# Kernel tuning notes

Measured on AMD Instinct MI355X. Metric: run time of the kernel, lower is better.

The kernel has to match this reference:

```python
import jax, jax.numpy as jnp
import numpy as np

H = 128  # lstm hidden

def _lstm_layer(x_tbi, Wih, Whh, bih, bhh):
    # x_tbi: [T, B, I]; Wih: [4H, I]; Whh: [4H, H]; biases: [4H]
    T, B, _ = x_tbi.shape
    b = bih + bhh
    # precompute input projections for all timesteps: [T, B, 4H]
    x_proj = jnp.einsum('tbi,gi->tbg', x_tbi, Wih) + b
    def step(carry, xp):
        h, c = carry
        gates = xp + h @ Whh.T  # [B, 4H]
        i, f, g, o = jnp.split(gates, 4, axis=-1)  # torch gate order i,f,g,o
        i = jax.nn.sigmoid(i); f = jax.nn.sigmoid(f)
        g = jnp.tanh(g); o = jax.nn.sigmoid(o)
        c = f * c + i * g
        h = o * jnp.tanh(c)
        return (h, c), h
    h0 = jnp.zeros((B, H), x_tbi.dtype)
    c0 = jnp.zeros((B, H), x_tbi.dtype)
    (_, _), hs = jax.lax.scan(step, (h0, c0), x_proj)
    return hs  # [T, B, H]


def setup_inputs() -> dict:
    key = jax.random.key(0)
    ks = jax.random.split(key, 14)
    B, T, I = 256, 512, 30
    k = 1.0 / np.sqrt(H)
    u = lambda kk, shape: jax.random.uniform(kk, shape, jnp.float32, -k, k)
    return {
        'x':    jax.random.normal(ks[0], (B, T, I), jnp.float32),
        'Wih0': u(ks[1], (4 * H, I)),
        'Whh0': u(ks[2], (4 * H, H)),
        'bih0': u(ks[3], (4 * H,)),
        'bhh0': u(ks[4], (4 * H,)),
        'Wih1': u(ks[5], (4 * H, H)),
        'Whh1': u(ks[6], (4 * H, H)),
        'bih1': u(ks[7], (4 * H,)),
        'bhh1': u(ks[8], (4 * H,)),
        'Wl':   u(ks[9], (84, H)),
        'bl':   u(ks[10], (84,)),
        'Wo':   u(ks[11], (63, 84)),
        'bo':   u(ks[12], (63,)),
    }


def reference(x, Wih0, Whh0, bih0, bhh0, Wih1, Whh1, bih1, bhh1, Wl, bl, Wo, bo):
    # x: [B, T, 30] -> time-major for scan
    x_tbi = jnp.swapaxes(x, 0, 1)
    h1 = _lstm_layer(x_tbi, Wih0, Whh0, bih0, bhh0)   # [T, B, H]
    h2 = _lstm_layer(h1,    Wih1, Whh1, bih1, bhh1)   # [T, B, H]
    y = jnp.swapaxes(h2, 0, 1)                         # [B, T, H]
    y = y @ Wl.T + bl                                  # [B, T, 84]
    out = y @ Wo.T + bo                                # [B, T, 63]
    return out
```

## Files before the change

kernel.cpp:

```cpp
#include <hip/hip_runtime.h>
#include <hip/hip_fp16.h>

#define B_ 256
#define T_ 512
#define H_ 128
#define M_ (B_ * T_)

typedef _Float16 f16x8 __attribute__((ext_vector_type(8)));
typedef float    f32x4 __attribute__((ext_vector_type(4)));

__device__ __forceinline__ float rcp_f(float a) { return __builtin_amdgcn_rcpf(a); }
__device__ __forceinline__ float sigmoid_f(float a) { return rcp_f(1.f + __expf(-a)); }
__device__ __forceinline__ float tanh_f(float a) { return 1.f - 2.f * rcp_f(__expf(2.f * a) + 1.f); }

__device__ __forceinline__ void lds_barrier() {
    asm volatile("s_waitcnt lgkmcnt(0)\n\ts_barrier" ::: "memory");
}

#define PINV(X) asm volatile("" : "+v"(X))

__device__ __forceinline__ __half cell_update(float g0, float g1, float g2, float g3, float& c) {
    float iv = sigmoid_f(g0), fv = sigmoid_f(g1);
    float gv = tanh_f(g2),   ov = sigmoid_f(g3);
    c = fv * c + iv * gv;
    return __float2half(ov * tanh_f(c));
}

__device__ __forceinline__ void store_dwordx2_sc(uint64_t addr, uint2 v) {
    asm volatile("global_store_dwordx2 %0, %1, off sc0 sc1" :: "v"(addr), "v"(v) : "memory");
}
__device__ __forceinline__ void store_flag_sc(uint64_t addr, unsigned v) {
    asm volatile("global_store_dword %0, %1, off sc0 sc1" :: "v"(addr), "v"(v) : "memory");
}
__device__ __forceinline__ unsigned load_flag_sc(uint64_t addr) {
    unsigned v;
    asm volatile("global_load_dword %0, %1, off sc0 sc1\n\ts_waitcnt vmcnt(0)"
                 : "=v"(v) : "v"(addr) : "memory");
    return v;
}
#define LOAD8_SC(dst, addr) \
    asm volatile("global_load_dwordx2 %0, %1, off sc0 sc1" : "=&v"(dst) : "v"(addr) : "memory")

__device__ __forceinline__ void poll_min8(uint64_t base, unsigned target, int lane) {
    for (;;) {
        unsigned v = 0xFFFFFFFFu;
        if (lane < 8) v = load_flag_sc(base + (uint64_t)lane * 4);
        v = min(v, (unsigned)__shfl_xor((int)v, 1));
        v = min(v, (unsigned)__shfl_xor((int)v, 2));
        v = min(v, (unsigned)__shfl_xor((int)v, 4));
        unsigned seen = (unsigned)__shfl((int)v, 0);
        if (seen >= target) break;
        __builtin_amdgcn_s_sleep(8);
    }
}

#define MFMA16(A, BV, C) __builtin_amdgcn_mfma_f32_16x16x32_f16((A), (BV), (C), 0, 0, 0)
#define MF4(AV, WARR, KT) \
    ac0 = MFMA16(AV, WARR[0][KT], ac0); \
    ac1 = MFMA16(AV, WARR[1][KT], ac1); \
    ac2 = MFMA16(AV, WARR[2][KT], ac2); \
    ac3 = MFMA16(AV, WARR[3][KT], ac3);
#define PF4(AV, KT) \
    px0 = MFMA16(AV, wi[0][KT], px0); \
    px1 = MFMA16(AV, wi[1][KT], px1); \
    px2 = MFMA16(AV, wi[2][KT], px2); \
    px3 = MFMA16(AV, wi[3][KT], px3);

__global__ __launch_bounds__(256)
void convert_kernel(const float* __restrict__ Wih0, const float* __restrict__ bih0, const float* __restrict__ bhh0,
                    const float* __restrict__ Whh0, const float* __restrict__ Wih1, const float* __restrict__ Whh1,
                    const float* __restrict__ bih1, const float* __restrict__ bhh1,
                    const float* __restrict__ Wl, const float* __restrict__ bl,
                    const float* __restrict__ Wo, const float* __restrict__ bo,
                    __half* __restrict__ W0b, __half* __restrict__ W1b,
                    __half* __restrict__ Whh0h, __half* __restrict__ Whh1h,
                    __half* __restrict__ Wc16, float* __restrict__ b0, float* __restrict__ b1,
                    float* __restrict__ bc)
{
    const int tid = threadIdx.x, bid = blockIdx.x;
    if (bid == 0) {
        for (int i = tid; i < 512; i += 256) { b0[i] = bih0[i] + bhh0[i]; b1[i] = bih1[i] + bhh1[i]; }
        for (int i = tid; i < 512 * 32; i += 256) {
            int r = i >> 5, k = i & 31;
            W0b[i] = __float2half(k < 30 ? Wih0[r * 30 + k] : 0.f);
        }
        if (tid < 64) {
            float a = 0.f;
            if (tid < 63) { a = bo[tid]; for (int m = 0; m < 84; ++m) a += Wo[tid * 84 + m] * bl[m]; }
            bc[tid] = a;
        }
    } else if (bid <= 4) {
        const int base = (bid - 1) * 16384;
        for (int i = tid; i < 16384; i += 256) W1b[base + i] = __float2half(Wih1[base + i]);
    } else if (bid <= 8) {
        const int base = (bid - 5) * 16384;
        for (int i = tid; i < 16384; i += 256) Whh0h[base + i] = __float2half(Whh0[base + i]);
    } else if (bid <= 12) {
        const int base = (bid - 9) * 16384;
        for (int i = tid; i < 16384; i += 256) Whh1h[base + i] = __float2half(Whh1[base + i]);
    } else {
        const int base = (bid - 13) * 2048;
        for (int i = tid; i < 2048; i += 256) {
            int idx = base + i;
            int j = idx >> 7, k = idx & 127;
            float a = 0.f;
            if (j < 63) for (int m = 0; m < 84; ++m) a += Wo[j * 84 + m] * Wl[m * 128 + k];
            Wc16[idx] = __float2half(a);
        }
    }
}

__global__ __launch_bounds__(512, 2)
void lstm_fused(const float* __restrict__ x,
                const __half* __restrict__ W0b, const __half* __restrict__ Whh0h,
                const __half* __restrict__ W1b, const __half* __restrict__ Whh1h,
                const float* __restrict__ b0, const float* __restrict__ b1,
                __half* __restrict__ xp, __half* __restrict__ h2g,
                unsigned* __restrict__ flags)
{
    const int bid = blockIdx.x;
    const bool producer = bid < 128;
    const int g = producer ? bid : bid - 128;
    const int tid = threadIdx.x;
    const int w = tid >> 6;
    const int lane = tid & 63;
    const int l15 = lane & 15, qg = lane >> 4;
    const int j = w * 16 + l15;
    const int r = l15 >> 2;

    __shared__ __align__(16) char hist[32 * 1280];
    __shared__ __align__(16) char hbuf_s[2][1280];
    __shared__ __align__(16) __half xl[2][129][32];
    char* const hb0 = hbuf_s[0];
    char* const hb1 = hbuf_s[1];

    const int ro0 = r * 320 + 0 * 64 + qg * 16;
    const int ro1 = r * 320 + 1 * 64 + qg * 16;
    const int ro2 = r * 320 + 2 * 64 + qg * 16;
    const int ro3 = r * 320 + 3 * 64 + qg * 16;
    const int wo  = qg * 320 + j * 2;

    for (int i = tid; i < 10240; i += 512) ((unsigned*)hist)[i] = 0;
    for (int i = tid; i < 320; i += 512) ((unsigned*)hb0)[i] = 0;

    const uint64_t fb = (uint64_t)(uintptr_t)flags;
    const uint64_t flagbase = fb + (uint64_t)(g * 8) * 4;
    float c = 0.f;

    if (producer) {
        float bias4[4], b14[4];
        f16x8 wx[4], wb[4][4], wi[4][4];
#pragma unroll
        for (int q = 0; q < 4; ++q) {
            bias4[q] = b0[q * 128 + j];
            b14[q]   = b1[q * 128 + j];
            wx[q] = *reinterpret_cast<const f16x8*>(W0b + (size_t)(q * 128 + j) * 32 + qg * 8);
            PINV(wx[q]); PINV(bias4[q]); PINV(b14[q]);
#pragma unroll
            for (int kt = 0; kt < 4; ++kt) {
                wb[q][kt] = *reinterpret_cast<const f16x8*>(Whh0h + (size_t)(q * 128 + j) * 128 + kt * 32 + qg * 8);
                wi[q][kt] = *reinterpret_cast<const f16x8*>(W1b   + (size_t)(q * 128 + j) * 128 + kt * 32 + qg * 8);
                PINV(wb[q][kt]); PINV(wi[q][kt]);
            }
        }
        for (int idx = tid; idx < 512; idx += 512) {
            int b4 = idx >> 8, rest = idx & 255;
            xl[b4][rest >> 1][30 + (rest & 1)] = __float2half(0.f);
        }
        if (tid < 512) {
            int idx = tid;
            if (idx < 512) {
                int b4 = idx >> 8, rest = idx & 255;
                xl[b4][rest >> 1][30 + (rest & 1)] = __float2half(0.f);
            }
        }
        const uint64_t pflag = flagbase + (uint64_t)w * 4;
        const uint64_t xpj = (uint64_t)(uintptr_t)xp + ((uint64_t)(4 * j) << 1);
        const char* xlb = (const char*)xl;
        const int xro = (r & 1) * 8256 + qg * 16;
        __syncthreads();

        auto xp1_gemm = [&](int cc2) {
#pragma unroll
            for (int rt = 0; rt < 4; ++rt) {
                const int row = rt * 16 + l15;
                const char* ap = hist + (((cc2 * 16 + (row >> 2)) & 31) * 1280 + (row & 3) * 320 + qg * 16);
                f16x8 h0_ = *(const f16x8*)(ap + 0);
                f16x8 h1_ = *(const f16x8*)(ap + 64);
                f16x8 h2_ = *(const f16x8*)(ap + 128);
                f16x8 h3_ = *(const f16x8*)(ap + 192);
                f32x4 px0 = (f32x4){b14[0], b14[0], b14[0], b14[0]};
                f32x4 px1 = (f32x4){b14[1], b14[1], b14[1], b14[1]};
                f32x4 px2 = (f32x4){b14[2], b14[2], b14[2], b14[2]};
                f32x4 px3 = (f32x4){b14[3], b14[3], b14[3], b14[3]};
                PF4(h0_, 0) PF4(h1_, 1) PF4(h2_, 2) PF4(h3_, 3)
#pragma unroll
                for (int r4 = 0; r4 < 4; ++r4) {
                    const int ro_ = rt * 16 + qg * 4 + r4;
                    const int tglob = cc2 * 16 + (ro_ >> 2);
                    const int b2 = ro_ & 3;
                    if (b2 < 2) {
                        __half2 lo_ = __floats2half2_rn(px0[r4], px1[r4]);
                        __half2 hi_ = __floats2half2_rn(px2[r4], px3[r4]);
                        uint2 pk_;
                        pk_.x = __builtin_bit_cast(unsigned, lo_);
                        pk_.y = __builtin_bit_cast(unsigned, hi_);
                        store_dwordx2_sc(xpj + ((uint64_t)((g * 2 + b2) * T_ + tglob) << 10), pk_);
                    }
                }
            }
        };

#define PSTEP(TT) do {                                                          \
        const int t_ = (TT);                                                    \
        const char* rp_ = hist + (((t_ + 31) & 31) * 1280);                     \
        f16x8 a0_ = *(const f16x8*)(rp_ + ro0);                                 \
        f16x8 a1_ = *(const f16x8*)(rp_ + ro1);                                 \
        f16x8 a2_ = *(const f16x8*)(rp_ + ro2);                                 \
        f16x8 a3_ = *(const f16x8*)(rp_ + ro3);                                 \
        f16x8 ax_ = *(const f16x8*)(xlb + (xro + (t_ & 127) * 64));             \
        f32x4 ac0 = (f32x4){bias4[0], 0.f, 0.f, 0.f};                           \
        f32x4 ac1 = (f32x4){bias4[1], 0.f, 0.f, 0.f};                           \
        f32x4 ac2 = (f32x4){bias4[2], 0.f, 0.f, 0.f};                           \
        f32x4 ac3 = (f32x4){bias4[3], 0.f, 0.f, 0.f};                           \
        ac0 = MFMA16(ax_, wx[0], ac0); ac1 = MFMA16(ax_, wx[1], ac1);           \
        ac2 = MFMA16(ax_, wx[2], ac2); ac3 = MFMA16(ax_, wx[3], ac3);           \
        MF4(a0_, wb, 0) MF4(a1_, wb, 1) MF4(a2_, wb, 2) MF4(a3_, wb, 3)         \
        __half hh_ = cell_update(ac0[0], ac1[0], ac2[0], ac3[0], c);            \
        *(__half*)(hist + ((t_ & 31) * 1280 + qg * 320 + j * 2)) = hh_;         \
        if ((t_ & 7) == 7) {                                                    \
            asm volatile("s_waitcnt vmcnt(0)" ::: "memory");                    \
            if (lane == 0) store_flag_sc(pflag, (unsigned)(t_ + 1));            \
        }                                                                       \
        lds_barrier();                                                          \
    } while (0)

        for (int xc = 0; xc < 4; ++xc) {
#pragma unroll 1
            for (int b4 = 0; b4 < 2; ++b4) {
                const float* src = x + ((size_t)(g * 2 + b4) * T_ + xc * 128) * 30;
                for (int idx = tid; idx < 3840; idx += 512) {
                    int tt = idx / 30, ii = idx - tt * 30;
                    xl[b4][tt][ii] = __float2half(src[idx]);
                }
            }
            __syncthreads();
#pragma unroll 1
            for (int sc = 0; sc < 8; ++sc) {
                const int cc = xc * 8 + sc;
                if (cc > 0) xp1_gemm(cc - 1);
                const int tb = cc * 16;
                PSTEP(tb + 0);  PSTEP(tb + 1);  PSTEP(tb + 2);  PSTEP(tb + 3);
                PSTEP(tb + 4);  PSTEP(tb + 5);  PSTEP(tb + 6);  PSTEP(tb + 7);
                PSTEP(tb + 8);  PSTEP(tb + 9);  PSTEP(tb + 10); PSTEP(tb + 11);
                PSTEP(tb + 12); PSTEP(tb + 13); PSTEP(tb + 14); PSTEP(tb + 15);
            }
        }
        xp1_gemm(31);
        asm volatile("s_waitcnt vmcnt(0)" ::: "memory");
        if (lane == 0) store_flag_sc(pflag, 999u);
    } else {
        f16x8 wb[4][4];
#pragma unroll
        for (int q = 0; q < 4; ++q)
#pragma unroll
            for (int kt = 0; kt < 4; ++kt) {
                wb[q][kt] = *reinterpret_cast<const f16x8*>(Whh1h + (size_t)(q * 128 + j) * 128 + kt * 32 + qg * 8);
                PINV(wb[q][kt]);
            }
        const int b = g * 2 + (qg & 1);
        const bool wrl = qg < 2;
        const uint64_t xpcb = (uint64_t)(uintptr_t)xp + ((uint64_t)(((size_t)b * T_) * 512 + 4 * j) << 1);
        __half* h2p = h2g + ((size_t)b * T_) * H_ + j;
        uint2 xq0, xq1, xq2, xq3, xq4, xq5, xq6, xq7;
        __syncthreads();

#define CSTEP(TT, XQ) do {                                                      \
        const int t_ = (TT);                                                    \
        const char* rp_ = (t_ & 1) ? hb1 : hb0;                                 \
        char* wp_ = (t_ & 1) ? hb0 : hb1;                                       \
        asm volatile("s_waitcnt vmcnt(15)" ::: "memory");                       \
        __builtin_amdgcn_sched_barrier(0);                                      \
        float2 flo = __half22float2(__builtin_bit_cast(__half2, XQ.x));         \
        float2 fhi = __half22float2(__builtin_bit_cast(__half2, XQ.y));         \
        LOAD8_SC(XQ, xpcb + (uint64_t)(t_ + 8) * 1024);                         \
        f16x8 a0_ = *(const f16x8*)(rp_ + ro0);                                 \
        f16x8 a1_ = *(const f16x8*)(rp_ + ro1);                                 \
        f16x8 a2_ = *(const f16x8*)(rp_ + ro2);                                 \
        f16x8 a3_ = *(const f16x8*)(rp_ + ro3);                                 \
        f32x4 ac0 = (f32x4){flo.x, 0.f, 0.f, 0.f};                              \
        f32x4 ac1 = (f32x4){flo.y, 0.f, 0.f, 0.f};                              \
        f32x4 ac2 = (f32x4){fhi.x, 0.f, 0.f, 0.f};                              \
        f32x4 ac3 = (f32x4){fhi.y, 0.f, 0.f, 0.f};                              \
        MF4(a0_, wb, 0) MF4(a1_, wb, 1) MF4(a2_, wb, 2) MF4(a3_, wb, 3)         \
        __half hh_ = cell_update(ac0[0], ac1[0], ac2[0], ac3[0], c);            \
        *(__half*)(wp_ + wo) = hh_;                                             \
        if (wrl) h2p[(size_t)t_ * H_] = hh_;                                    \
        lds_barrier();                                                          \
    } while (0)

        for (int tg = 0; tg < T_; tg += 16) {
            unsigned target = (tg + 40 <= 512) ? (unsigned)(tg + 40) : 999u;
            poll_min8(flagbase, target, lane);
            if (tg == 0) {
                LOAD8_SC(xq0, xpcb + 0 * 1024); LOAD8_SC(xq1, xpcb + 1 * 1024);
                LOAD8_SC(xq2, xpcb + 2 * 1024); LOAD8_SC(xq3, xpcb + 3 * 1024);
                LOAD8_SC(xq4, xpcb + 4 * 1024); LOAD8_SC(xq5, xpcb + 5 * 1024);
                LOAD8_SC(xq6, xpcb + 6 * 1024); LOAD8_SC(xq7, xpcb + 7 * 1024);
                asm volatile("s_waitcnt vmcnt(0)" ::: "memory");
                __builtin_amdgcn_sched_barrier(0);
            }
            CSTEP(tg + 0, xq0);  CSTEP(tg + 1, xq1);  CSTEP(tg + 2, xq2);  CSTEP(tg + 3, xq3);
            CSTEP(tg + 4, xq4);  CSTEP(tg + 5, xq5);  CSTEP(tg + 6, xq6);  CSTEP(tg + 7, xq7);
            CSTEP(tg + 8, xq0);  CSTEP(tg + 9, xq1);  CSTEP(tg + 10, xq2); CSTEP(tg + 11, xq3);
            CSTEP(tg + 12, xq4); CSTEP(tg + 13, xq5); CSTEP(tg + 14, xq6); CSTEP(tg + 15, xq7);
        }
    }
}

__global__ __launch_bounds__(256, 4)
void head_kernel(const __half* __restrict__ in, const __half* __restrict__ W16,
                 const float* __restrict__ bias, float* __restrict__ outp)
{
    constexpr int KK = 128;
    const int lane = threadIdx.x & 63;
    const int wn = threadIdx.x >> 6;
    const int rowbase = blockIdx.x * 64;
    const int colbase = wn * 16;
    const int l15 = lane & 15, lk = (lane >> 4) * 8;

    float bcol = bias[colbase + l15];
    f32x4 acc[4];
#pragma unroll
    for (int rt = 0; rt < 4; ++rt) acc[rt] = (f32x4){0.f, 0.f, 0.f, 0.f};

#pragma unroll
    for (int kt = 0; kt < 4; ++kt) {
        f16x8 bv = *reinterpret_cast<const f16x8*>(W16 + (size_t)(colbase + l15) * KK + kt * 32 + lk);
#pragma unroll
        for (int rt = 0; rt < 4; ++rt) {
            f16x8 a = *reinterpret_cast<const f16x8*>(in + (size_t)(rowbase + rt * 16 + l15) * KK + kt * 32 + lk);
            acc[rt] = __builtin_amdgcn_mfma_f32_16x16x32_f16(a, bv, acc[rt], 0, 0, 0);
        }
    }
    const int col = colbase + l15;
#pragma unroll
    for (int rt = 0; rt < 4; ++rt)
#pragma unroll
        for (int rr = 0; rr < 4; ++rr) {
            const int row = rowbase + rt * 16 + (lane >> 4) * 4 + rr;
            if (col < 63) outp[(size_t)row * 63 + col] = acc[rt][rr] + bcol;
        }
}

extern "C" void kernel_launch(void* const* d_in, const int* in_sizes, int n_in,
                              void* d_out, int out_size, void* d_ws, size_t ws_size,
                              hipStream_t stream)
{
    const float* x    = (const float*)d_in[0];
    const float* Wih0 = (const float*)d_in[1];
    const float* Whh0 = (const float*)d_in[2];
    const float* bih0 = (const float*)d_in[3];
    const float* bhh0 = (const float*)d_in[4];
    const float* Wih1 = (const float*)d_in[5];
    const float* Whh1 = (const float*)d_in[6];
    const float* bih1 = (const float*)d_in[7];
    const float* bhh1 = (const float*)d_in[8];
    const float* Wl   = (const float*)d_in[9];
    const float* bl   = (const float*)d_in[10];
    const float* Wo   = (const float*)d_in[11];
    const float* bo   = (const float*)d_in[12];
    float* out = (float*)d_out;

    char* ws = (char*)d_ws;
    size_t off = 0;
    auto carve = [&](size_t bytes) { void* p = ws + off; off += (bytes + 255) & ~(size_t)255; return p; };
    __half* xp    = (__half*)carve((size_t)M_ * 512 * 2 + 16384);
    __half* h2    = (__half*)carve((size_t)M_ * 128 * 2);
    __half* W0b   = (__half*)carve(512 * 32 * 2);
    __half* W1b   = (__half*)carve(512 * 128 * 2);
    __half* Whh0h = (__half*)carve(512 * 128 * 2);
    __half* Whh1h = (__half*)carve(512 * 128 * 2);
    __half* Wc16  = (__half*)carve(64 * 128 * 2);
    float*  b0    = (float*)carve(512 * 4);
    float*  b1    = (float*)carve(512 * 4);
    float*  bc    = (float*)carve(64 * 4);
    unsigned* flags = (unsigned*)carve(2048 * 4);

    hipLaunchKernelGGL(convert_kernel, dim3(17), dim3(256), 0, stream,
                       Wih0, bih0, bhh0, Whh0, Wih1, Whh1, bih1, bhh1, Wl, bl, Wo, bo,
                       W0b, W1b, Whh0h, Whh1h, Wc16, b0, b1, bc);

    hipMemsetAsync(flags, 0, 2048 * 4, stream);

    hipLaunchKernelGGL(lstm_fused, dim3(256), dim3(512), 0, stream,
                       x, W0b, Whh0h, W1b, Whh1h, b0, b1, xp, h2, flags);

    hipLaunchKernelGGL(head_kernel, dim3(M_ / 64), dim3(256), 0, stream,
                       h2, Wc16, bc, out);
}
```

Before: 364.0 us.

## Precompute layer-0 input projection for step pairs ahead, shrink hidden history ring

```diff
diff --git a/kernel.cpp b/kernel.cpp
--- a/kernel.cpp
+++ b/kernel.cpp
@@ -128,9 +128,10 @@
     const int j = w * 16 + l15;
     const int r = l15 >> 2;
 
-    __shared__ __align__(16) char hist[32 * 1280];
+    __shared__ __align__(16) char hist[16 * 1280];
     __shared__ __align__(16) char hbuf_s[2][1280];
     __shared__ __align__(16) __half xl[2][129][32];
+    __shared__ __align__(16) char gb0[2 * 8 * 1040];
     char* const hb0 = hbuf_s[0];
     char* const hb1 = hbuf_s[1];
 
@@ -140,7 +141,7 @@
     const int ro3 = r * 320 + 3 * 64 + qg * 16;
     const int wo  = qg * 320 + j * 2;
 
-    for (int i = tid; i < 10240; i += 512) ((unsigned*)hist)[i] = 0;
+    for (int i = tid; i < 5120; i += 512) ((unsigned*)hist)[i] = 0;
     for (int i = tid; i < 320; i += 512) ((unsigned*)hb0)[i] = 0;
 
     const uint64_t fb = (uint64_t)(uintptr_t)flags;
@@ -167,24 +168,17 @@
             int b4 = idx >> 8, rest = idx & 255;
             xl[b4][rest >> 1][30 + (rest & 1)] = __float2half(0.f);
         }
-        if (tid < 512) {
-            int idx = tid;
-            if (idx < 512) {
-                int b4 = idx >> 8, rest = idx & 255;
-                xl[b4][rest >> 1][30 + (rest & 1)] = __float2half(0.f);
-            }
-        }
         const uint64_t pflag = flagbase + (uint64_t)w * 4;
         const uint64_t xpj = (uint64_t)(uintptr_t)xp + ((uint64_t)(4 * j) << 1);
         const char* xlb = (const char*)xl;
-        const int xro = (r & 1) * 8256 + qg * 16;
         __syncthreads();
 
         auto xp1_gemm = [&](int cc2) {
 #pragma unroll
-            for (int rt = 0; rt < 4; ++rt) {
+            for (int rt = 0; rt < 2; ++rt) {
                 const int row = rt * 16 + l15;
-                const char* ap = hist + (((cc2 * 16 + (row >> 2)) & 31) * 1280 + (row & 3) * 320 + qg * 16);
+                const int s_ = row >> 1, b2_ = row & 1;
+                const char* ap = hist + (((cc2 * 16 + s_) & 15) * 1280 + b2_ * 320 + qg * 16);
                 f16x8 h0_ = *(const f16x8*)(ap + 0);
                 f16x8 h1_ = *(const f16x8*)(ap + 64);
                 f16x8 h2_ = *(const f16x8*)(ap + 128);
@@ -197,42 +191,68 @@
 #pragma unroll
                 for (int r4 = 0; r4 < 4; ++r4) {
                     const int ro_ = rt * 16 + qg * 4 + r4;
-                    const int tglob = cc2 * 16 + (ro_ >> 2);
-                    const int b2 = ro_ & 3;
-                    if (b2 < 2) {
-                        __half2 lo_ = __floats2half2_rn(px0[r4], px1[r4]);
-                        __half2 hi_ = __floats2half2_rn(px2[r4], px3[r4]);
-                        uint2 pk_;
-                        pk_.x = __builtin_bit_cast(unsigned, lo_);
-                        pk_.y = __builtin_bit_cast(unsigned, hi_);
-                        store_dwordx2_sc(xpj + ((uint64_t)((g * 2 + b2) * T_ + tglob) << 10), pk_);
-                    }
+                    const int s2 = ro_ >> 1, b2 = ro_ & 1;
+                    __half2 lo_ = __floats2half2_rn(px0[r4], px1[r4]);
+                    __half2 hi_ = __floats2half2_rn(px2[r4], px3[r4]);
+                    uint2 pk_;
+                    pk_.x = __builtin_bit_cast(unsigned, lo_);
+                    pk_.y = __builtin_bit_cast(unsigned, hi_);
+                    store_dwordx2_sc(xpj + ((uint64_t)((g * 2 + b2) * T_ + cc2 * 16 + s2) << 10), pk_);
                 }
             }
         };
+
+#define XP0B(CC) do {                                                           \
+        const int sl_ = (l15 >> 2) & 1, bb_ = l15 & 1;                          \
+        f16x8 ax_ = *(const f16x8*)(xlb + bb_ * 8256 + ((((CC) * 2 + sl_) & 127) * 64) + qg * 16); \
+        f32x4 px0 = (f32x4){bias4[0], bias4[0], bias4[0], bias4[0]};            \
+        f32x4 px1 = (f32x4){bias4[1], bias4[1], bias4[1], bias4[1]};            \
+        f32x4 px2 = (f32x4){bias4[2], bias4[2], bias4[2], bias4[2]};            \
+        f32x4 px3 = (f32x4){bias4[3], bias4[3], bias4[3], bias4[3]};            \
+        px0 = MFMA16(ax_, wx[0], px0); px1 = MFMA16(ax_, wx[1], px1);           \
+        px2 = MFMA16(ax_, wx[2], px2); px3 = MFMA16(ax_, wx[3], px3);           \
+        char* gd_ = gb0 + ((CC) & 1) * 8320 + 8 * j;                            \
+        _Pragma("unroll")                                                       \
+        for (int r4 = 0; r4 < 2; ++r4) {                                        \
+            const int grow_ = (qg & 1) * 4 + (qg >> 1) * 2 + r4;                \
+            __half2 lo_ = __floats2half2_rn(px0[r4], px1[r4]);                  \
+            __half2 hi_ = __floats2half2_rn(px2[r4], px3[r4]);                  \
+            uint2 pk_;                                                          \
+            pk_.x = __builtin_bit_cast(unsigned, lo_);                          \
+            pk_.y = __builtin_bit_cast(unsigned, hi_);                          \
+            *(uint2*)(gd_ + grow_ * 1040) = pk_;                                \
+        }                                                                       \
+    } while (0)
 
 #define PSTEP(TT) do {                                                          \
         const int t_ = (TT);                                                    \
-        const char* rp_ = hist + (((t_ + 31) & 31) * 1280);                     \
+        const char* rp_ = hist + (((t_ + 15) & 15) * 1280);                     \
+        const char* gq_ = gb0 + (((t_ >> 1) & 1) * 8320) + (((t_ & 1) * 4 + qg) * 1040) + 8 * j; \
+        uint2 xq_ = *(const uint2*)gq_;                                         \
         f16x8 a0_ = *(const f16x8*)(rp_ + ro0);                                 \
         f16x8 a1_ = *(const f16x8*)(rp_ + ro1);                                 \
         f16x8 a2_ = *(const f16x8*)(rp_ + ro2);                                 \
         f16x8 a3_ = *(const f16x8*)(rp_ + ro3);                                 \
-        f16x8 ax_ = *(const f16x8*)(xlb + (xro + (t_ & 127) * 64));             \
-        f32x4 ac0 = (f32x4){bias4[0], 0.f, 0.f, 0.f};                           \
-        f32x4 ac1 = (f32x4){bias4[1], 0.f, 0.f, 0.f};                           \
-        f32x4 ac2 = (f32x4){bias4[2], 0.f, 0.f, 0.f};                           \
-        f32x4 ac3 = (f32x4){bias4[3], 0.f, 0.f, 0.f};                           \
-        ac0 = MFMA16(ax_, wx[0], ac0); ac1 = MFMA16(ax_, wx[1], ac1);           \
-        ac2 = MFMA16(ax_, wx[2], ac2); ac3 = MFMA16(ax_, wx[3], ac3);           \
+        float2 flo = __half22float2(__builtin_bit_cast(__half2, xq_.x));        \
+        float2 fhi = __half22float2(__builtin_bit_cast(__half2, xq_.y));        \
+        f32x4 ac0 = (f32x4){flo.x, 0.f, 0.f, 0.f};                              \
+        f32x4 ac1 = (f32x4){flo.y, 0.f, 0.f, 0.f};                              \
+        f32x4 ac2 = (f32x4){fhi.x, 0.f, 0.f, 0.f};                              \
+        f32x4 ac3 = (f32x4){fhi.y, 0.f, 0.f, 0.f};                              \
         MF4(a0_, wb, 0) MF4(a1_, wb, 1) MF4(a2_, wb, 2) MF4(a3_, wb, 3)         \
         __half hh_ = cell_update(ac0[0], ac1[0], ac2[0], ac3[0], c);            \
-        *(__half*)(hist + ((t_ & 31) * 1280 + qg * 320 + j * 2)) = hh_;         \
+        *(__half*)(hist + ((t_ & 15) * 1280 + qg * 320 + j * 2)) = hh_;         \
         if ((t_ & 7) == 7) {                                                    \
             asm volatile("s_waitcnt vmcnt(0)" ::: "memory");                    \
             if (lane == 0) store_flag_sc(pflag, (unsigned)(t_ + 1));            \
         }                                                                       \
         lds_barrier();                                                          \
+    } while (0)
+
+#define PAIR(K) do {                                                            \
+        const int te_ = tb + (K);                                               \
+        if (te_ + 2 < 512 && ((te_) & 127) != 126) XP0B((te_ >> 1) + 1);        \
+        PSTEP(te_); PSTEP(te_ + 1);                                             \
     } while (0)
 
         for (int xc = 0; xc < 4; ++xc) {
@@ -245,15 +265,15 @@
                 }
             }
             __syncthreads();
+            XP0B(xc * 64);
+            lds_barrier();
 #pragma unroll 1
             for (int sc = 0; sc < 8; ++sc) {
                 const int cc = xc * 8 + sc;
                 if (cc > 0) xp1_gemm(cc - 1);
                 const int tb = cc * 16;
-                PSTEP(tb + 0);  PSTEP(tb + 1);  PSTEP(tb + 2);  PSTEP(tb + 3);
-                PSTEP(tb + 4);  PSTEP(tb + 5);  PSTEP(tb + 6);  PSTEP(tb + 7);
-                PSTEP(tb + 8);  PSTEP(tb + 9);  PSTEP(tb + 10); PSTEP(tb + 11);
-                PSTEP(tb + 12); PSTEP(tb + 13); PSTEP(tb + 14); PSTEP(tb + 15);
+                PAIR(0);  PAIR(2);  PAIR(4);  PAIR(6);
+                PAIR(8);  PAIR(10); PAIR(12); PAIR(14);
             }
         }
         xp1_gemm(31);
```

Result: faster. 356.6 us (-2.0%).
